# Kernel optimization log

Measured on AMD Instinct MI355X. Metric: run time of the kernel, lower is better.

The kernel has to match this reference:

```python
import jax, jax.numpy as jnp
import numpy as np

HIDDEN_DIM = 256
Z_DIM = 64
B = 8
SRC_LEN = 2048
NUM_DIRS = 2


def setup_inputs() -> dict:
    key = jax.random.key(0)
    ks = jax.random.split(key, 7)
    return {
        "encoder_hidden_state": jax.random.normal(ks[0], (NUM_DIRS, B, HIDDEN_DIM), dtype=jnp.float32),
        "decoder_hidden_state": jax.random.normal(ks[1], (B, HIDDEN_DIM), dtype=jnp.float32),
        "latent_z_seq": jax.random.normal(ks[2], (B, SRC_LEN, Z_DIM), dtype=jnp.float32),
        "mask": jax.random.randint(ks[3], (B, SRC_LEN), 0, 2, dtype=jnp.int32),
        "weight_q": jax.random.normal(ks[4], (HIDDEN_DIM + Z_DIM, HIDDEN_DIM), dtype=jnp.float32),
        "weight_k": jax.random.normal(ks[5], (HIDDEN_DIM + Z_DIM, HIDDEN_DIM), dtype=jnp.float32),
        "weight_v": jax.random.normal(ks[6], (HIDDEN_DIM + Z_DIM, HIDDEN_DIM), dtype=jnp.float32),
    }


def reference(encoder_hidden_state, decoder_hidden_state, latent_z_seq, mask,
              weight_q, weight_k, weight_v):
    # decoder_hidden_state is accepted but unused (as in the original forward).
    src_len = latent_z_seq.shape[1]
    temperature = jnp.asarray(HIDDEN_DIM ** 0.5, latent_z_seq.dtype)
    # sum over directions/layers: [D,B,H] -> [B,H], broadcast along seq
    enc = jnp.sum(encoder_hidden_state, axis=0)  # [B,H]
    enc = jnp.broadcast_to(enc[:, None, :], (enc.shape[0], src_len, enc.shape[1]))
    attn_input = jnp.concatenate((enc, latent_z_seq), axis=2)  # [B,S,H+Z]
    q = jnp.einsum('bsd,dh->bsh', attn_input, weight_q)
    k = jnp.einsum('bsd,dh->bsh', attn_input, weight_k)
    v = jnp.einsum('bsd,dh->bsh', attn_input, weight_v)
    scores = jnp.einsum('bqh,bkh->bqk', q, k) / temperature  # [B,S,S]
    # mask[:, :, None] broadcasts along the key axis (masks query rows)
    scores = jnp.where(mask[:, :, None] == 0, jnp.asarray(-1e9, scores.dtype), scores)
    attn = jax.nn.softmax(scores, axis=-1)
    output = jnp.einsum('bqk,bkh->bqh', attn, v)  # [B,S,H]
    return (output, attn)
```

## Files before the change

### kernel.cpp

```cpp
#include <hip/hip_runtime.h>
#include <hip/hip_bf16.h>

#define B_ 8
#define S_ 2048
#define H_ 256
#define Z_ 64
#define CHK 32
#define NQCH 16
#define BS (B_*S_)

typedef short bf16x8 __attribute__((ext_vector_type(8)));
typedef float f32x4 __attribute__((ext_vector_type(4)));

__device__ __forceinline__ unsigned short f2bf(float f) {
  __hip_bfloat16 h = __float2bfloat16(f);
  return *reinterpret_cast<unsigned short*>(&h);
}
__device__ __forceinline__ float bf2f(unsigned short u) {
  __hip_bfloat16 h;
  *reinterpret_cast<unsigned short*>(&h) = u;
  return __bfloat162float(h);
}

__device__ __forceinline__ void gl_lds16(const void* g, void* l) {
  __builtin_amdgcn_global_load_lds(
      (const __attribute__((address_space(1))) unsigned int*)(uintptr_t)g,
      (__attribute__((address_space(3))) unsigned int*)(uintptr_t)l,
      16, 0, 0);
}

__global__ __launch_bounds__(256) void k0_base(
    const float* __restrict__ enc, const float* __restrict__ Wq,
    const float* __restrict__ Wk, const float* __restrict__ Wv,
    float* __restrict__ q0, float* __restrict__ k0, float* __restrict__ v0) {
  int b = blockIdx.x;
  int h = threadIdx.x;
  __shared__ float encs[H_];
  encs[h] = enc[b*H_ + h] + enc[B_*H_ + b*H_ + h];
  __syncthreads();
  float aq = 0.f, ak = 0.f, av = 0.f;
  #pragma unroll 4
  for (int d = 0; d < H_; d++) {
    float e = encs[d];
    aq = fmaf(e, Wq[d*H_ + h], aq);
    ak = fmaf(e, Wk[d*H_ + h], ak);
    av = fmaf(e, Wv[d*H_ + h], av);
  }
  q0[b*H_ + h] = aq;
  k0[b*H_ + h] = ak;
  v0[b*H_ + h] = av;
}

__global__ __launch_bounds__(256) void k1_prep(
    const float* __restrict__ z, const float* __restrict__ Wq,
    const float* __restrict__ Wk, const float* __restrict__ Wv,
    const float* __restrict__ q0, const float* __restrict__ k0b, const float* __restrict__ v0,
    unsigned short* __restrict__ Qhi, unsigned short* __restrict__ Qlo,
    unsigned short* __restrict__ Khi, unsigned short* __restrict__ Klo,
    unsigned short* __restrict__ Vt) {
  int b  = blockIdx.x >> 7;
  int st = blockIdx.x & 127;
  int tid = threadIdx.x;
  __shared__ float zs[16*Z_];
  __shared__ float vbuf[16][H_];
  {
    const float4* zp = reinterpret_cast<const float4*>(z + ((size_t)b*S_ + st*16)*Z_);
    reinterpret_cast<float4*>(zs)[tid] = zp[tid];
  }
  __syncthreads();
  float bq = q0[b*H_ + tid], bk = k0b[b*H_ + tid], bv = v0[b*H_ + tid];
  float accq[16], acck[16], accv[16];
  #pragma unroll
  for (int s = 0; s < 16; s++) { accq[s] = bq; acck[s] = bk; accv[s] = bv; }
  #pragma unroll 2
  for (int z0 = 0; z0 < Z_; z0 += 8) {
    float wq[8], wk[8], wv[8];
    #pragma unroll
    for (int j = 0; j < 8; j++) {
      wq[j] = Wq[(H_+z0+j)*H_ + tid];
      wk[j] = Wk[(H_+z0+j)*H_ + tid];
      wv[j] = Wv[(H_+z0+j)*H_ + tid];
    }
    #pragma unroll
    for (int j = 0; j < 8; j++) {
      #pragma unroll
      for (int s = 0; s < 16; s++) {
        float zz = zs[s*Z_ + z0 + j];
        accq[s] = fmaf(zz, wq[j], accq[s]);
        acck[s] = fmaf(zz, wk[j], acck[s]);
        accv[s] = fmaf(zz, wv[j], accv[s]);
      }
    }
  }
  #pragma unroll
  for (int s = 0; s < 16; s++) {
    size_t row = ((size_t)b*S_ + st*16 + s)*H_ + tid;
    unsigned short qh = f2bf(accq[s]);
    Qhi[row] = qh;
    Qlo[row] = f2bf(accq[s] - bf2f(qh));
    unsigned short kh = f2bf(acck[s]);
    Khi[row] = kh;
    Klo[row] = f2bf(acck[s] - bf2f(kh));
    vbuf[s][tid] = accv[s];
  }
  __syncthreads();
  unsigned int pk[8];
  #pragma unroll
  for (int j = 0; j < 8; j++) {
    pk[j] = (unsigned int)f2bf(vbuf[2*j][tid]) |
            ((unsigned int)f2bf(vbuf[2*j+1][tid]) << 16);
  }
  uint4* vt4 = reinterpret_cast<uint4*>(Vt + ((size_t)b*H_ + tid)*S_ + st*16);
  vt4[0] = make_uint4(pk[0], pk[1], pk[2], pk[3]);
  vt4[1] = make_uint4(pk[4], pk[5], pk[6], pk[7]);
}

__global__ __launch_bounds__(256, 2) void k2_flash(
    const unsigned short* __restrict__ Qhi, const unsigned short* __restrict__ Qlo,
    const unsigned short* __restrict__ Khi, const unsigned short* __restrict__ Klo,
    const unsigned short* __restrict__ Vt, const int* __restrict__ mask,
    float* __restrict__ attn, float* __restrict__ Mq, float* __restrict__ Lq,
    unsigned short* __restrict__ Opart) {
  int bb    = blockIdx.x;
  int b     = bb & 7;
  int strip = (bb >> 3) & 31;
  int kq    = bb >> 8;
  int qb    = strip*64;
  int k0q   = kq*512;
  int tid  = threadIdx.x;
  int wave = tid >> 6;
  int lane = tid & 63;
  int l15  = lane & 15;
  int quad = lane >> 4;
  int qw   = qb + wave*16;

  __shared__ __align__(16) unsigned short KhiL[32*256];
  __shared__ __align__(16) unsigned short KloL[32*256];
  __shared__ __align__(16) unsigned short VtL[256*32];
  __shared__ __align__(16) unsigned short Ps[4][16*32];

  const unsigned short* KhiB = Khi + (size_t)b*S_*H_;
  const unsigned short* KloB = Klo + (size_t)b*S_*H_;
  const unsigned short* VtB  = Vt  + (size_t)b*H_*S_;

  int sub = lane >> 5;
  int c5  = lane & 31;
  int hl  = lane >> 2;
  int jj  = lane & 3;

  auto dma_chunk = [&](int c) {
    int kc = k0q + c*CHK;
    #pragma unroll
    for (int t = 0; t < 4; t++) {
      int i = wave*4 + t;
      int row = i*2 + sub;
      size_t gs = (size_t)(kc + row)*H_ + ((c5 ^ row)*8);
      gl_lds16(KhiB + gs, &KhiL[i*512]);
      gl_lds16(KloB + gs, &KloL[i*512]);
    }
    #pragma unroll
    for (int t = 0; t < 4; t++) {
      int i = wave*4 + t;
      int h = i*16 + hl;
      gl_lds16(VtB + (size_t)h*S_ + kc + jj*8, &VtL[i*512]);
    }
  };

  bf16x8 qh[8], ql[8];
  {
    const unsigned short* qhp = Qhi + ((size_t)b*S_ + qw + l15)*H_ + quad*8;
    const unsigned short* qlp = Qlo + ((size_t)b*S_ + qw + l15)*H_ + quad*8;
    #pragma unroll
    for (int dc = 0; dc < 8; dc++) {
      qh[dc] = *reinterpret_cast<const bf16x8*>(qhp + dc*32);
      ql[dc] = *reinterpret_cast<const bf16x8*>(qlp + dc*32);
    }
  }
  int mrow[4];
  #pragma unroll
  for (int r = 0; r < 4; r++) mrow[r] = mask[b*S_ + qw + quad*4 + r];

  f32x4 acc_o[16];
  #pragma unroll
  for (int ht = 0; ht < 16; ht++) acc_o[ht] = (f32x4){0.f, 0.f, 0.f, 0.f};
  float m_run[4] = {-1e30f, -1e30f, -1e30f, -1e30f};
  float l_run[4] = {0.f, 0.f, 0.f, 0.f};

  dma_chunk(0);
  __syncthreads();

  for (int c = 0; c < NQCH; c++) {
    int kc = k0q + c*CHK;
    f32x4 sacc[2];
    #pragma unroll
    for (int kt = 0; kt < 2; kt++) {
      int row = kt*16 + l15;
      const unsigned short* khb = &KhiL[row*256];
      const unsigned short* klb = &KloL[row*256];
      f32x4 a0 = (f32x4){0.f, 0.f, 0.f, 0.f};
      f32x4 a1 = (f32x4){0.f, 0.f, 0.f, 0.f};
      #pragma unroll
      for (int dc = 0; dc < 8; dc += 2) {
        int s0 = ((dc*4 + quad) ^ row) * 8;
        int s1 = (((dc+1)*4 + quad) ^ row) * 8;
        bf16x8 kh0 = *reinterpret_cast<const bf16x8*>(khb + s0);
        bf16x8 kl0 = *reinterpret_cast<const bf16x8*>(klb + s0);
        bf16x8 kh1 = *reinterpret_cast<const bf16x8*>(khb + s1);
        bf16x8 kl1 = *reinterpret_cast<const bf16x8*>(klb + s1);
        a0 = __builtin_amdgcn_mfma_f32_16x16x32_bf16(qh[dc], kh0, a0, 0, 0, 0);
        a1 = __builtin_amdgcn_mfma_f32_16x16x32_bf16(qh[dc+1], kh1, a1, 0, 0, 0);
        a0 = __builtin_amdgcn_mfma_f32_16x16x32_bf16(ql[dc], kh0, a0, 0, 0, 0);
        a1 = __builtin_amdgcn_mfma_f32_16x16x32_bf16(ql[dc+1], kh1, a1, 0, 0, 0);
        a0 = __builtin_amdgcn_mfma_f32_16x16x32_bf16(qh[dc], kl0, a0, 0, 0, 0);
        a1 = __builtin_amdgcn_mfma_f32_16x16x32_bf16(qh[dc+1], kl1, a1, 0, 0, 0);
      }
      sacc[kt] = a0 + a1;
    }
    float p[2][4], alpha[4], se[2][4];
    #pragma unroll
    for (int r = 0; r < 4; r++) {
      se[0][r] = mrow[r] ? sacc[0][r]*0.0625f : -1e9f;
      se[1][r] = mrow[r] ? sacc[1][r]*0.0625f : -1e9f;
      float ml = fmaxf(se[0][r], se[1][r]);
      ml = fmaxf(ml, __shfl_xor(ml, 1));
      ml = fmaxf(ml, __shfl_xor(ml, 2));
      ml = fmaxf(ml, __shfl_xor(ml, 4));
      ml = fmaxf(ml, __shfl_xor(ml, 8));
      float mnew = fmaxf(m_run[r], ml);
      alpha[r] = __expf(m_run[r] - mnew);
      p[0][r] = __expf(se[0][r] - mnew);
      p[1][r] = __expf(se[1][r] - mnew);
      float ls = p[0][r] + p[1][r];
      ls += __shfl_xor(ls, 1);
      ls += __shfl_xor(ls, 2);
      ls += __shfl_xor(ls, 4);
      ls += __shfl_xor(ls, 8);
      l_run[r] = l_run[r]*alpha[r] + ls;
      m_run[r] = mnew;
    }
    #pragma unroll
    for (int ht = 0; ht < 16; ht++) {
      acc_o[ht][0] *= alpha[0];
      acc_o[ht][1] *= alpha[1];
      acc_o[ht][2] *= alpha[2];
      acc_o[ht][3] *= alpha[3];
    }
    #pragma unroll
    for (int kt = 0; kt < 2; kt++) {
      #pragma unroll
      for (int r = 0; r < 4; r++) {
        attn[((size_t)b*S_ + qw + quad*4 + r)*S_ + kc + kt*16 + l15] = se[kt][r];
        Ps[wave][(quad*4 + r)*32 + kt*16 + l15] = f2bf(p[kt][r]);
      }
    }
    bf16x8 pa = *reinterpret_cast<const bf16x8*>(&Ps[wave][l15*32 + quad*8]);
    #pragma unroll
    for (int ht = 0; ht < 16; ht++) {
      bf16x8 v = *reinterpret_cast<const bf16x8*>(&VtL[(ht*16 + l15)*32 + quad*8]);
      acc_o[ht] = __builtin_amdgcn_mfma_f32_16x16x32_bf16(pa, v, acc_o[ht], 0, 0, 0);
    }
    __syncthreads();
    if (c+1 < NQCH) {
      dma_chunk(c+1);
      __syncthreads();
    }
  }

  if (l15 == 0) {
    #pragma unroll
    for (int r = 0; r < 4; r++) {
      int idx = kq*BS + b*S_ + qw + quad*4 + r;
      Mq[idx] = m_run[r];
      Lq[idx] = l_run[r];
    }
  }
  #pragma unroll
  for (int ht = 0; ht < 16; ht++) {
    #pragma unroll
    for (int r = 0; r < 4; r++) {
      size_t idx = ((size_t)kq*BS + b*S_ + qw + quad*4 + r)*H_ + ht*16 + l15;
      Opart[idx] = f2bf(acc_o[ht][r]);
    }
  }
}

__global__ __launch_bounds__(256) void k3_combine(
    const float* __restrict__ Mq, const float* __restrict__ Lq,
    const unsigned short* __restrict__ Opart,
    float* __restrict__ attn, float* __restrict__ outp) {
  int gr  = blockIdx.x;
  int tid = threadIdx.x;
  float m0 = Mq[gr], m1 = Mq[BS + gr], m2 = Mq[2*BS + gr], m3 = Mq[3*BS + gr];
  float m = fmaxf(fmaxf(m0, m1), fmaxf(m2, m3));
  float e0 = __expf(m0 - m), e1 = __expf(m1 - m);
  float e2 = __expf(m2 - m), e3 = __expf(m3 - m);
  float l = Lq[gr]*e0 + Lq[BS + gr]*e1 + Lq[2*BS + gr]*e2 + Lq[3*BS + gr]*e3;
  float il = 1.f / l;
  float o = e0*bf2f(Opart[(size_t)gr*H_ + tid])
          + e1*bf2f(Opart[((size_t)BS + gr)*H_ + tid])
          + e2*bf2f(Opart[((size_t)2*BS + gr)*H_ + tid])
          + e3*bf2f(Opart[((size_t)3*BS + gr)*H_ + tid]);
  outp[(size_t)gr*H_ + tid] = o * il;
  float4* pa = reinterpret_cast<float4*>(attn + (size_t)gr*S_ + tid*8);
  float4 x0 = pa[0], x1 = pa[1];
  x0.x = __expf(x0.x - m)*il; x0.y = __expf(x0.y - m)*il;
  x0.z = __expf(x0.z - m)*il; x0.w = __expf(x0.w - m)*il;
  x1.x = __expf(x1.x - m)*il; x1.y = __expf(x1.y - m)*il;
  x1.z = __expf(x1.z - m)*il; x1.w = __expf(x1.w - m)*il;
  pa[0] = x0; pa[1] = x1;
}

extern "C" void kernel_launch(void* const* d_in, const int* in_sizes, int n_in,
                              void* d_out, int out_size, void* d_ws, size_t ws_size,
                              hipStream_t stream) {
  const float* enc = (const float*)d_in[0];
  const float* z   = (const float*)d_in[2];
  const int* mask  = (const int*)d_in[3];
  const float* Wq  = (const float*)d_in[4];
  const float* Wk  = (const float*)d_in[5];
  const float* Wv  = (const float*)d_in[6];

  char* ws = (char*)d_ws;
  const size_t MB = 1024*1024;
  unsigned short* Qhi = (unsigned short*)(ws);
  unsigned short* Qlo = (unsigned short*)(ws +  8*MB);
  unsigned short* Khi = (unsigned short*)(ws + 16*MB);
  unsigned short* Klo = (unsigned short*)(ws + 24*MB);
  unsigned short* Vt  = (unsigned short*)(ws + 32*MB);
  float* q0 = (float*)(ws + 40*MB);
  float* k0 = q0 + B_*H_;
  float* v0 = k0 + B_*H_;
  float* Mq = (float*)(ws + 41*MB);
  float* Lq = (float*)(ws + 41*MB + 512*1024);
  unsigned short* Opart = (unsigned short*)(ws + 42*MB);

  float* outp = (float*)d_out;
  float* attn = outp + (size_t)B_*S_*H_;

  k0_base<<<B_, 256, 0, stream>>>(enc, Wq, Wk, Wv, q0, k0, v0);
  k1_prep<<<B_*(S_/16), 256, 0, stream>>>(z, Wq, Wk, Wv, q0, k0, v0,
                                          Qhi, Qlo, Khi, Klo, Vt);
  k2_flash<<<B_*(S_/64)*4, 256, 0, stream>>>(Qhi, Qlo, Khi, Klo, Vt, mask,
                                             attn, Mq, Lq, Opart);
  k3_combine<<<B_*S_, 256, 0, stream>>>(Mq, Lq, Opart, attn, outp);
}
```

Measured before the change: 365.9 us.

## Double-buffer K/V chunks, widen query tile per wave, move row-sum to combine

New measurement: 385.1 us. 5.2% more time.

```diff
diff --git a/kernel.cpp b/kernel.cpp
--- a/kernel.cpp
+++ b/kernel.cpp
@@ -8,6 +8,7 @@
 #define CHK 32
 #define NQCH 16
 #define BS (B_*S_)
+#define PSLD 40
 
 typedef short bf16x8 __attribute__((ext_vector_type(8)));
 typedef float f32x4 __attribute__((ext_vector_type(4)));
@@ -115,29 +116,29 @@
   vt4[1] = make_uint4(pk[4], pk[5], pk[6], pk[7]);
 }
 
-__global__ __launch_bounds__(256, 2) void k2_flash(
+__global__ __launch_bounds__(256, 1) void k2_flash(
     const unsigned short* __restrict__ Qhi, const unsigned short* __restrict__ Qlo,
     const unsigned short* __restrict__ Khi, const unsigned short* __restrict__ Klo,
     const unsigned short* __restrict__ Vt, const int* __restrict__ mask,
-    float* __restrict__ attn, float* __restrict__ Mq, float* __restrict__ Lq,
+    float* __restrict__ attn, float* __restrict__ Mq,
     unsigned short* __restrict__ Opart) {
   int bb    = blockIdx.x;
   int b     = bb & 7;
-  int strip = (bb >> 3) & 31;
-  int kq    = bb >> 8;
-  int qb    = strip*64;
+  int strip = (bb >> 3) & 15;
+  int kq    = bb >> 7;
+  int qb    = strip*128;
   int k0q   = kq*512;
   int tid  = threadIdx.x;
   int wave = tid >> 6;
   int lane = tid & 63;
   int l15  = lane & 15;
   int quad = lane >> 4;
-  int qw   = qb + wave*16;
-
-  __shared__ __align__(16) unsigned short KhiL[32*256];
-  __shared__ __align__(16) unsigned short KloL[32*256];
-  __shared__ __align__(16) unsigned short VtL[256*32];
-  __shared__ __align__(16) unsigned short Ps[4][16*32];
+  int qw   = qb + wave*32;
+
+  __shared__ __align__(16) unsigned short KhiL[2][32*256];
+  __shared__ __align__(16) unsigned short KloL[2][32*256];
+  __shared__ __align__(16) unsigned short VtL[2][256*32];
+  __shared__ __align__(16) unsigned short Ps[4][2][16*PSLD];
 
   const unsigned short* KhiB = Khi + (size_t)b*S_*H_;
   const unsigned short* KloB = Klo + (size_t)b*S_*H_;
@@ -149,56 +150,67 @@
   int jj  = lane & 3;
 
   auto dma_chunk = [&](int c) {
+    int buf = c & 1;
     int kc = k0q + c*CHK;
     #pragma unroll
     for (int t = 0; t < 4; t++) {
       int i = wave*4 + t;
       int row = i*2 + sub;
       size_t gs = (size_t)(kc + row)*H_ + ((c5 ^ row)*8);
-      gl_lds16(KhiB + gs, &KhiL[i*512]);
-      gl_lds16(KloB + gs, &KloL[i*512]);
+      gl_lds16(KhiB + gs, &KhiL[buf][i*512]);
+      gl_lds16(KloB + gs, &KloL[buf][i*512]);
     }
     #pragma unroll
     for (int t = 0; t < 4; t++) {
       int i = wave*4 + t;
       int h = i*16 + hl;
-      gl_lds16(VtB + (size_t)h*S_ + kc + jj*8, &VtL[i*512]);
+      gl_lds16(VtB + (size_t)h*S_ + kc + ((jj ^ (hl & 3))*8), &VtL[buf][i*512]);
     }
   };
 
-  bf16x8 qh[8], ql[8];
-  {
-    const unsigned short* qhp = Qhi + ((size_t)b*S_ + qw + l15)*H_ + quad*8;
-    const unsigned short* qlp = Qlo + ((size_t)b*S_ + qw + l15)*H_ + quad*8;
+  bf16x8 qh[2][8], ql[2][8];
+  #pragma unroll
+  for (int qt = 0; qt < 2; qt++) {
+    const unsigned short* qhp = Qhi + ((size_t)b*S_ + qw + qt*16 + l15)*H_ + quad*8;
+    const unsigned short* qlp = Qlo + ((size_t)b*S_ + qw + qt*16 + l15)*H_ + quad*8;
     #pragma unroll
     for (int dc = 0; dc < 8; dc++) {
-      qh[dc] = *reinterpret_cast<const bf16x8*>(qhp + dc*32);
-      ql[dc] = *reinterpret_cast<const bf16x8*>(qlp + dc*32);
-    }
-  }
-  int mrow[4];
-  #pragma unroll
-  for (int r = 0; r < 4; r++) mrow[r] = mask[b*S_ + qw + quad*4 + r];
-
-  f32x4 acc_o[16];
-  #pragma unroll
-  for (int ht = 0; ht < 16; ht++) acc_o[ht] = (f32x4){0.f, 0.f, 0.f, 0.f};
-  float m_run[4] = {-1e30f, -1e30f, -1e30f, -1e30f};
-  float l_run[4] = {0.f, 0.f, 0.f, 0.f};
+      qh[qt][dc] = *reinterpret_cast<const bf16x8*>(qhp + dc*32);
+      ql[qt][dc] = *reinterpret_cast<const bf16x8*>(qlp + dc*32);
+    }
+  }
+  int mrow[2][4];
+  #pragma unroll
+  for (int qt = 0; qt < 2; qt++)
+    #pragma unroll
+    for (int r = 0; r < 4; r++) mrow[qt][r] = mask[b*S_ + qw + qt*16 + quad*4 + r];
+
+  f32x4 acc_o[2][16];
+  #pragma unroll
+  for (int qt = 0; qt < 2; qt++)
+    #pragma unroll
+    for (int ht = 0; ht < 16; ht++) acc_o[qt][ht] = (f32x4){0.f, 0.f, 0.f, 0.f};
+  float m_run[2][4] = {{-1e30f,-1e30f,-1e30f,-1e30f},{-1e30f,-1e30f,-1e30f,-1e30f}};
 
   dma_chunk(0);
   __syncthreads();
 
   for (int c = 0; c < NQCH; c++) {
-    int kc = k0q + c*CHK;
-    f32x4 sacc[2];
+    if (c+1 < NQCH) dma_chunk(c+1);
+    int buf = c & 1;
+    int kc  = k0q + c*CHK;
+    f32x4 sacc[2][2];
     #pragma unroll
     for (int kt = 0; kt < 2; kt++) {
       int row = kt*16 + l15;
-      const unsigned short* khb = &KhiL[row*256];
-      const unsigned short* klb = &KloL[row*256];
-      f32x4 a0 = (f32x4){0.f, 0.f, 0.f, 0.f};
-      f32x4 a1 = (f32x4){0.f, 0.f, 0.f, 0.f};
+      const unsigned short* khb = &KhiL[buf][row*256];
+      const unsigned short* klb = &KloL[buf][row*256];
+      f32x4 a0[2], a1[2];
+      #pragma unroll
+      for (int qt = 0; qt < 2; qt++) {
+        a0[qt] = (f32x4){0.f,0.f,0.f,0.f};
+        a1[qt] = (f32x4){0.f,0.f,0.f,0.f};
+      }
       #pragma unroll
       for (int dc = 0; dc < 8; dc += 2) {
         int s0 = ((dc*4 + quad) ^ row) * 8;
@@ -207,107 +219,120 @@
         bf16x8 kl0 = *reinterpret_cast<const bf16x8*>(klb + s0);
         bf16x8 kh1 = *reinterpret_cast<const bf16x8*>(khb + s1);
         bf16x8 kl1 = *reinterpret_cast<const bf16x8*>(klb + s1);
-        a0 = __builtin_amdgcn_mfma_f32_16x16x32_bf16(qh[dc], kh0, a0, 0, 0, 0);
-        a1 = __builtin_amdgcn_mfma_f32_16x16x32_bf16(qh[dc+1], kh1, a1, 0, 0, 0);
-        a0 = __builtin_amdgcn_mfma_f32_16x16x32_bf16(ql[dc], kh0, a0, 0, 0, 0);
-        a1 = __builtin_amdgcn_mfma_f32_16x16x32_bf16(ql[dc+1], kh1, a1, 0, 0, 0);
-        a0 = __builtin_amdgcn_mfma_f32_16x16x32_bf16(qh[dc], kl0, a0, 0, 0, 0);
-        a1 = __builtin_amdgcn_mfma_f32_16x16x32_bf16(qh[dc+1], kl1, a1, 0, 0, 0);
-      }
-      sacc[kt] = a0 + a1;
-    }
-    float p[2][4], alpha[4], se[2][4];
-    #pragma unroll
-    for (int r = 0; r < 4; r++) {
-      se[0][r] = mrow[r] ? sacc[0][r]*0.0625f : -1e9f;
-      se[1][r] = mrow[r] ? sacc[1][r]*0.0625f : -1e9f;
-      float ml = fmaxf(se[0][r], se[1][r]);
-      ml = fmaxf(ml, __shfl_xor(ml, 1));
-      ml = fmaxf(ml, __shfl_xor(ml, 2));
-      ml = fmaxf(ml, __shfl_xor(ml, 4));
-      ml = fmaxf(ml, __shfl_xor(ml, 8));
-      float mnew = fmaxf(m_run[r], ml);
-      alpha[r] = __expf(m_run[r] - mnew);
-      p[0][r] = __expf(se[0][r] - mnew);
-      p[1][r] = __expf(se[1][r] - mnew);
-      float ls = p[0][r] + p[1][r];
-      ls += __shfl_xor(ls, 1);
-      ls += __shfl_xor(ls, 2);
-      ls += __shfl_xor(ls, 4);
-      ls += __shfl_xor(ls, 8);
-      l_run[r] = l_run[r]*alpha[r] + ls;
-      m_run[r] = mnew;
-    }
+        #pragma unroll
+        for (int qt = 0; qt < 2; qt++) {
+          a0[qt] = __builtin_amdgcn_mfma_f32_16x16x32_bf16(qh[qt][dc],   kh0, a0[qt], 0, 0, 0);
+          a1[qt] = __builtin_amdgcn_mfma_f32_16x16x32_bf16(qh[qt][dc+1], kh1, a1[qt], 0, 0, 0);
+          a0[qt] = __builtin_amdgcn_mfma_f32_16x16x32_bf16(ql[qt][dc],   kh0, a0[qt], 0, 0, 0);
+          a1[qt] = __builtin_amdgcn_mfma_f32_16x16x32_bf16(ql[qt][dc+1], kh1, a1[qt], 0, 0, 0);
+          a0[qt] = __builtin_amdgcn_mfma_f32_16x16x32_bf16(qh[qt][dc],   kl0, a0[qt], 0, 0, 0);
+          a1[qt] = __builtin_amdgcn_mfma_f32_16x16x32_bf16(qh[qt][dc+1], kl1, a1[qt], 0, 0, 0);
+        }
+      }
+      #pragma unroll
+      for (int qt = 0; qt < 2; qt++) sacc[qt][kt] = a0[qt] + a1[qt];
+    }
+    float p[2][2][4], alpha[2][4];
+    bool resc = false;
+    #pragma unroll
+    for (int qt = 0; qt < 2; qt++) {
+      #pragma unroll
+      for (int r = 0; r < 4; r++) {
+        float se0 = mrow[qt][r] ? sacc[qt][0][r]*0.0625f : -1e9f;
+        float se1 = mrow[qt][r] ? sacc[qt][1][r]*0.0625f : -1e9f;
+        float ml = fmaxf(se0, se1);
+        ml = fmaxf(ml, __shfl_xor(ml, 1));
+        ml = fmaxf(ml, __shfl_xor(ml, 2));
+        ml = fmaxf(ml, __shfl_xor(ml, 4));
+        ml = fmaxf(ml, __shfl_xor(ml, 8));
+        float mnew = fmaxf(m_run[qt][r], ml);
+        alpha[qt][r] = __expf(m_run[qt][r] - mnew);
+        p[qt][0][r] = __expf(se0 - mnew);
+        p[qt][1][r] = __expf(se1 - mnew);
+        m_run[qt][r] = mnew;
+        resc |= (alpha[qt][r] < 1.f);
+        attn[((size_t)b*S_ + qw + qt*16 + quad*4 + r)*S_ + kc + l15]      = se0;
+        attn[((size_t)b*S_ + qw + qt*16 + quad*4 + r)*S_ + kc + 16 + l15] = se1;
+      }
+    }
+    if (__any(resc)) {
+      #pragma unroll
+      for (int qt = 0; qt < 2; qt++)
+        #pragma unroll
+        for (int ht = 0; ht < 16; ht++) {
+          acc_o[qt][ht][0] *= alpha[qt][0];
+          acc_o[qt][ht][1] *= alpha[qt][1];
+          acc_o[qt][ht][2] *= alpha[qt][2];
+          acc_o[qt][ht][3] *= alpha[qt][3];
+        }
+    }
+    #pragma unroll
+    for (int qt = 0; qt < 2; qt++)
+      #pragma unroll
+      for (int kt = 0; kt < 2; kt++)
+        #pragma unroll
+        for (int r = 0; r < 4; r++)
+          Ps[wave][qt][(quad*4 + r)*PSLD + kt*16 + l15] = f2bf(p[qt][kt][r]);
+    bf16x8 pa0 = *reinterpret_cast<const bf16x8*>(&Ps[wave][0][l15*PSLD + quad*8]);
+    bf16x8 pa1 = *reinterpret_cast<const bf16x8*>(&Ps[wave][1][l15*PSLD + quad*8]);
     #pragma unroll
     for (int ht = 0; ht < 16; ht++) {
-      acc_o[ht][0] *= alpha[0];
-      acc_o[ht][1] *= alpha[1];
-      acc_o[ht][2] *= alpha[2];
-      acc_o[ht][3] *= alpha[3];
-    }
-    #pragma unroll
-    for (int kt = 0; kt < 2; kt++) {
+      bf16x8 v = *reinterpret_cast<const bf16x8*>(
+          &VtL[buf][(ht*16 + l15)*32 + ((quad ^ (l15 & 3))*8)]);
+      acc_o[0][ht] = __builtin_amdgcn_mfma_f32_16x16x32_bf16(pa0, v, acc_o[0][ht], 0, 0, 0);
+      acc_o[1][ht] = __builtin_amdgcn_mfma_f32_16x16x32_bf16(pa1, v, acc_o[1][ht], 0, 0, 0);
+    }
+    __syncthreads();
+  }
+
+  if (l15 == 0) {
+    #pragma unroll
+    for (int qt = 0; qt < 2; qt++)
+      #pragma unroll
+      for (int r = 0; r < 4; r++)
+        Mq[kq*BS + b*S_ + qw + qt*16 + quad*4 + r] = m_run[qt][r];
+  }
+  #pragma unroll
+  for (int qt = 0; qt < 2; qt++)
+    #pragma unroll
+    for (int ht = 0; ht < 16; ht++)
       #pragma unroll
       for (int r = 0; r < 4; r++) {
-        attn[((size_t)b*S_ + qw + quad*4 + r)*S_ + kc + kt*16 + l15] = se[kt][r];
-        Ps[wave][(quad*4 + r)*32 + kt*16 + l15] = f2bf(p[kt][r]);
-      }
-    }
-    bf16x8 pa = *reinterpret_cast<const bf16x8*>(&Ps[wave][l15*32 + quad*8]);
-    #pragma unroll
-    for (int ht = 0; ht < 16; ht++) {
-      bf16x8 v = *reinterpret_cast<const bf16x8*>(&VtL[(ht*16 + l15)*32 + quad*8]);
-      acc_o[ht] = __builtin_amdgcn_mfma_f32_16x16x32_bf16(pa, v, acc_o[ht], 0, 0, 0);
-    }
-    __syncthreads();
-    if (c+1 < NQCH) {
-      dma_chunk(c+1);
-      __syncthreads();
-    }
-  }
-
-  if (l15 == 0) {
-    #pragma unroll
-    for (int r = 0; r < 4; r++) {
-      int idx = kq*BS + b*S_ + qw + quad*4 + r;
-      Mq[idx] = m_run[r];
-      Lq[idx] = l_run[r];
-    }
-  }
-  #pragma unroll
-  for (int ht = 0; ht < 16; ht++) {
-    #pragma unroll
-    for (int r = 0; r < 4; r++) {
-      size_t idx = ((size_t)kq*BS + b*S_ + qw + quad*4 + r)*H_ + ht*16 + l15;
-      Opart[idx] = f2bf(acc_o[ht][r]);
-    }
-  }
+        size_t idx = ((size_t)kq*BS + b*S_ + qw + qt*16 + quad*4 + r)*H_ + ht*16 + l15;
+        Opart[idx] = f2bf(acc_o[qt][ht][r]);
+      }
 }
 
 __global__ __launch_bounds__(256) void k3_combine(
-    const float* __restrict__ Mq, const float* __restrict__ Lq,
-    const unsigned short* __restrict__ Opart,
+    const float* __restrict__ Mq, const unsigned short* __restrict__ Opart,
     float* __restrict__ attn, float* __restrict__ outp) {
   int gr  = blockIdx.x;
   int tid = threadIdx.x;
+  int lane = tid & 63, wv = tid >> 6;
+  __shared__ float red[4];
   float m0 = Mq[gr], m1 = Mq[BS + gr], m2 = Mq[2*BS + gr], m3 = Mq[3*BS + gr];
   float m = fmaxf(fmaxf(m0, m1), fmaxf(m2, m3));
-  float e0 = __expf(m0 - m), e1 = __expf(m1 - m);
-  float e2 = __expf(m2 - m), e3 = __expf(m3 - m);
-  float l = Lq[gr]*e0 + Lq[BS + gr]*e1 + Lq[2*BS + gr]*e2 + Lq[3*BS + gr]*e3;
-  float il = 1.f / l;
-  float o = e0*bf2f(Opart[(size_t)gr*H_ + tid])
-          + e1*bf2f(Opart[((size_t)BS + gr)*H_ + tid])
-          + e2*bf2f(Opart[((size_t)2*BS + gr)*H_ + tid])
-          + e3*bf2f(Opart[((size_t)3*BS + gr)*H_ + tid]);
-  outp[(size_t)gr*H_ + tid] = o * il;
   float4* pa = reinterpret_cast<float4*>(attn + (size_t)gr*S_ + tid*8);
   float4 x0 = pa[0], x1 = pa[1];
-  x0.x = __expf(x0.x - m)*il; x0.y = __expf(x0.y - m)*il;
-  x0.z = __expf(x0.z - m)*il; x0.w = __expf(x0.w - m)*il;
-  x1.x = __expf(x1.x - m)*il; x1.y = __expf(x1.y - m)*il;
-  x1.z = __expf(x1.z - m)*il; x1.w = __expf(x1.w - m)*il;
+  x0.x = __expf(x0.x - m); x0.y = __expf(x0.y - m);
+  x0.z = __expf(x0.z - m); x0.w = __expf(x0.w - m);
+  x1.x = __expf(x1.x - m); x1.y = __expf(x1.y - m);
+  x1.z = __expf(x1.z - m); x1.w = __expf(x1.w - m);
+  float ps = x0.x + x0.y + x0.z + x0.w + x1.x + x1.y + x1.z + x1.w;
+  ps += __shfl_xor(ps, 1);  ps += __shfl_xor(ps, 2);
+  ps += __shfl_xor(ps, 4);  ps += __shfl_xor(ps, 8);
+  ps += __shfl_xor(ps, 16); ps += __shfl_xor(ps, 32);
+  if (lane == 0) red[wv] = ps;
+  __syncthreads();
+  float il = 1.f / (red[0] + red[1] + red[2] + red[3]);
+  x0.x *= il; x0.y *= il; x0.z *= il; x0.w *= il;
+  x1.x *= il; x1.y *= il; x1.z *= il; x1.w *= il;
   pa[0] = x0; pa[1] = x1;
+  float o = __expf(m0 - m)*bf2f(Opart[(size_t)gr*H_ + tid])
+          + __expf(m1 - m)*bf2f(Opart[((size_t)BS + gr)*H_ + tid])
+          + __expf(m2 - m)*bf2f(Opart[((size_t)2*BS + gr)*H_ + tid])
+          + __expf(m3 - m)*bf2f(Opart[((size_t)3*BS + gr)*H_ + tid]);
+  outp[(size_t)gr*H_ + tid] = o * il;
 }
 
 extern "C" void kernel_launch(void* const* d_in, const int* in_sizes, int n_in,
@@ -331,7 +356,6 @@
   float* k0 = q0 + B_*H_;
   float* v0 = k0 + B_*H_;
   float* Mq = (float*)(ws + 41*MB);
-  float* Lq = (float*)(ws + 41*MB + 512*1024);
   unsigned short* Opart = (unsigned short*)(ws + 42*MB);
 
   float* outp = (float*)d_out;
@@ -340,7 +364,7 @@
   k0_base<<<B_, 256, 0, stream>>>(enc, Wq, Wk, Wv, q0, k0, v0);
   k1_prep<<<B_*(S_/16), 256, 0, stream>>>(z, Wq, Wk, Wv, q0, k0, v0,
                                           Qhi, Qlo, Khi, Klo, Vt);
-  k2_flash<<<B_*(S_/64)*4, 256, 0, stream>>>(Qhi, Qlo, Khi, Klo, Vt, mask,
-                                             attn, Mq, Lq, Opart);
-  k3_combine<<<B_*S_, 256, 0, stream>>>(Mq, Lq, Opart, attn, outp);
-}
+  k2_flash<<<B_*(S_/128)*4, 256, 0, stream>>>(Qhi, Qlo, Khi, Klo, Vt, mask,
+                                              attn, Mq, Opart);
+  k3_combine<<<B_*S_, 256, 0, stream>>>(Mq, Opart, attn, outp);
+}
```
